# Kernel tuning notes

Hardware: AMD Instinct MI355X
Metric: run time of the kernel (lower is better)

## Reference

```python
import jax, jax.numpy as jnp
import numpy as np

NUM_LATENTS = 32768
NUM_EMBEDDINGS = 1024
EMBEDDING_SIZE = 64


def setup_inputs() -> dict:
    key = jax.random.key(0)
    kx, ke = jax.random.split(key)
    x = jax.random.normal(kx, (NUM_LATENTS * EMBEDDING_SIZE,), dtype=jnp.float32)
    # uniform init in [-limit, limit], limit = sqrt(3/embedding_size) as in the torch module
    limit = float(np.sqrt(3.0 / EMBEDDING_SIZE))
    embeddings = jax.random.uniform(
        ke, (NUM_EMBEDDINGS, EMBEDDING_SIZE), dtype=jnp.float32,
        minval=-limit, maxval=limit)
    return {"x": x, "embeddings": embeddings}


def reference(x, embeddings):
    K, E = embeddings.shape
    x_ = x.reshape(-1, E)  # [L, E]
    # squared distances ||x - e||^2 expanded: faithful to sum((x-e)**2, -1), fused as one GEMM
    d = (
        jnp.sum(x_ * x_, axis=-1, keepdims=True)
        - 2.0 * jnp.einsum('le,ke->lk', x_, embeddings)
        + jnp.sum(embeddings * embeddings, axis=-1)
    )  # [L, K]
    indices = jnp.argmin(d, axis=-1)          # [L]
    quantized = embeddings[indices].reshape(-1)  # [L*E]
    # straight-through estimator: x + (q - stop_grad(x))
    z_hat = x + quantized - jax.lax.stop_gradient(x)
    # outputs mirror the torch dict: z_continuous, z_quantized, z_hat, z_indices
    return x, quantized, z_hat, indices
```

## Files before the change

### kernel.cpp

```cpp
#include <hip/hip_runtime.h>

#define L_TOTAL   32768
#define E_DIM     64
#define K_TOTAL   1024
#define NT_TOTAL  64
#define OUT_STRIDE 2097152
#define XPAD      68

#define NT_WORDS  1280

typedef _Float16 half_t;
typedef _Float16 half8  __attribute__((ext_vector_type(8)));
typedef float    floatx4 __attribute__((ext_vector_type(4)));

__global__ __launch_bounds__(128)
void vq_swizzle_kernel(const float* __restrict__ emb, float* __restrict__ ebuf) {
    __shared__ float s_p[128];
    __shared__ float s_n[16];
    const int nt   = blockIdx.x;
    const int t    = threadIdx.x;
    const int kt   = t >> 6;
    const int lane = t & 63;
    const int q    = lane >> 4;
    const int ln   = lane & 15;

    const float* src = emb + (size_t)(nt * 16 + ln) * E_DIM + kt * 32 + q * 8;
    float4 v0 = *(const float4*)src;
    float4 v1 = *(const float4*)(src + 4);
    float f[8] = {v0.x, v0.y, v0.z, v0.w, v1.x, v1.y, v1.z, v1.w};

    half8 h, l;
    float s = 0.f;
    #pragma unroll
    for (int j = 0; j < 8; ++j) {
        half_t hh = (half_t)f[j];
        half_t ll = (half_t)(f[j] - (float)hh);
        h[j] = hh;
        l[j] = ll;
        s = fmaf(f[j], f[j], s);
    }
    float* rec = ebuf + (size_t)nt * NT_WORDS;
    *(half8*)(rec + kt * 256 + lane * 4)       = h;
    *(half8*)(rec + 512 + kt * 256 + lane * 4) = l;

    s_p[t] = s;
    __syncthreads();
    if (t < 16) {
        float n = 0.f;
        #pragma unroll
        for (int u = 0; u < 8; ++u)
            n += s_p[(u >> 2) * 64 + (u & 3) * 16 + t];
        s_n[t] = n;
    }
    __syncthreads();
    if (t < 64) rec[1024 + t] = s_n[t & 15];
}

__global__ __launch_bounds__(256, 4)
void vq_fused_kernel(const float* __restrict__ x,
                     const float* __restrict__ emb,
                     const float* __restrict__ ebuf,
                     float* __restrict__ out) {
    __shared__ float s_x[32 * XPAD];
    __shared__ float s_best[4][32];
    __shared__ int   s_bidx[4][32];
    __shared__ int   s_fin[32];

    const int tid   = threadIdx.x;
    const int ks    = tid >> 6;
    const int lane  = tid & 63;
    const int q     = lane >> 4;
    const int ln    = lane & 15;
    const int mbase = blockIdx.x * 32;
    const int rot   = blockIdx.x & 15;
    const int nt0   = ks * 16;

    {
        const float4* xg = (const float4*)(x + (size_t)mbase * E_DIM);
        #pragma unroll
        for (int i = 0; i < 2; ++i) {
            const int f   = i * 256 + tid;
            const int row = f >> 4;
            const int col = (f & 15) * 4;
            *(float4*)(&s_x[row * XPAD + col]) = xg[f];
        }
    }
    __syncthreads();

    half8 A[2][2][2];
    floatx4 xq[2];
    #pragma unroll
    for (int rt = 0; rt < 2; ++rt) {
        const float* xr = &s_x[(rt * 16 + ln) * XPAD + q * 8];
        float sn = 0.f;
        #pragma unroll
        for (int kt = 0; kt < 2; ++kt) {
            float4 v0 = *(const float4*)(xr + kt * 32);
            float4 v1 = *(const float4*)(xr + kt * 32 + 4);
            float f[8] = {v0.x, v0.y, v0.z, v0.w, v1.x, v1.y, v1.z, v1.w};
            #pragma unroll
            for (int j = 0; j < 8; ++j) {
                half_t hh = (half_t)f[j];
                half_t ll = (half_t)(f[j] - (float)hh);
                A[rt][kt][0][j] = hh;
                A[rt][kt][1][j] = ll;
                sn = fmaf(f[j], f[j], sn);
            }
        }
        sn += __shfl_xor(sn, 16, 64);
        sn += __shfl_xor(sn, 32, 64);
        #pragma unroll
        for (int r = 0; r < 4; ++r)
            xq[rt][r] = __shfl(sn, q * 4 + r, 64);
    }

    float best[2][4];
    int   bidx[2][4];
    #pragma unroll
    for (int rt = 0; rt < 2; ++rt)
        #pragma unroll
        for (int r = 0; r < 4; ++r) { best[rt][r] = 3.402823466e+38f; bidx[rt][r] = 0x7fffffff; }

    half8 a0, a1, a2, a3; float ae;
    half8 b0, b1, b2, b3; float be;
    int nt_a, nt_b;
    {
        nt_a = nt0 + rot;
        nt_a = nt0 + (rot & 15);
        nt_a = nt0 + ((0 + rot) & 15);
        const float* rec = ebuf + (size_t)nt_a * NT_WORDS;
        a0 = *(const half8*)(rec + lane * 4);
        a1 = *(const half8*)(rec + 256 + lane * 4);
        a2 = *(const half8*)(rec + 512 + lane * 4);
        a3 = *(const half8*)(rec + 768 + lane * 4);
        ae = rec[1024 + lane];
    }

    #pragma unroll 1
    for (int j = 0; j < 16; j += 2) {
        nt_b = nt0 + ((j + 1 + rot) & 15);
        {
            const float* rec = ebuf + (size_t)nt_b * NT_WORDS;
            b0 = *(const half8*)(rec + lane * 4);
            b1 = *(const half8*)(rec + 256 + lane * 4);
            b2 = *(const half8*)(rec + 512 + lane * 4);
            b3 = *(const half8*)(rec + 768 + lane * 4);
            be = rec[1024 + lane];
        }
        {
            const int kg = nt_a * 16 + ln;
            #pragma unroll
            for (int rt = 0; rt < 2; ++rt) {
                floatx4 Ca = {0.f, 0.f, 0.f, 0.f};
                floatx4 Cb = {0.f, 0.f, 0.f, 0.f};
                Ca = __builtin_amdgcn_mfma_f32_16x16x32_f16(A[rt][0][0], a0, Ca, 0, 0, 0);
                Ca = __builtin_amdgcn_mfma_f32_16x16x32_f16(A[rt][1][0], a1, Ca, 0, 0, 0);
                Cb = __builtin_amdgcn_mfma_f32_16x16x32_f16(A[rt][0][1], a0, Cb, 0, 0, 0);
                Cb = __builtin_amdgcn_mfma_f32_16x16x32_f16(A[rt][1][1], a1, Cb, 0, 0, 0);
                Cb = __builtin_amdgcn_mfma_f32_16x16x32_f16(A[rt][0][0], a2, Cb, 0, 0, 0);
                Cb = __builtin_amdgcn_mfma_f32_16x16x32_f16(A[rt][1][0], a3, Cb, 0, 0, 0);
                #pragma unroll
                for (int r = 0; r < 4; ++r) {
                    float dot = Ca[r] + Cb[r];
                    float d = __fadd_rn(__fsub_rn(xq[rt][r], __fmul_rn(2.0f, dot)), ae);
                    if (d < best[rt][r] || (d == best[rt][r] && kg < bidx[rt][r])) {
                        best[rt][r] = d; bidx[rt][r] = kg;
                    }
                }
            }
        }
        if (j + 2 < 16) {
            nt_a = nt0 + ((j + 2 + rot) & 15);
            const float* rec = ebuf + (size_t)nt_a * NT_WORDS;
            a0 = *(const half8*)(rec + lane * 4);
            a1 = *(const half8*)(rec + 256 + lane * 4);
            a2 = *(const half8*)(rec + 512 + lane * 4);
            a3 = *(const half8*)(rec + 768 + lane * 4);
            ae = rec[1024 + lane];
        }
        {
            const int kg = nt_b * 16 + ln;
            #pragma unroll
            for (int rt = 0; rt < 2; ++rt) {
                floatx4 Ca = {0.f, 0.f, 0.f, 0.f};
                floatx4 Cb = {0.f, 0.f, 0.f, 0.f};
                Ca = __builtin_amdgcn_mfma_f32_16x16x32_f16(A[rt][0][0], b0, Ca, 0, 0, 0);
                Ca = __builtin_amdgcn_mfma_f32_16x16x32_f16(A[rt][1][0], b1, Ca, 0, 0, 0);
                Cb = __builtin_amdgcn_mfma_f32_16x16x32_f16(A[rt][0][1], b0, Cb, 0, 0, 0);
                Cb = __builtin_amdgcn_mfma_f32_16x16x32_f16(A[rt][1][1], b1, Cb, 0, 0, 0);
                Cb = __builtin_amdgcn_mfma_f32_16x16x32_f16(A[rt][0][0], b2, Cb, 0, 0, 0);
                Cb = __builtin_amdgcn_mfma_f32_16x16x32_f16(A[rt][1][0], b3, Cb, 0, 0, 0);
                #pragma unroll
                for (int r = 0; r < 4; ++r) {
                    float dot = Ca[r] + Cb[r];
                    float d = __fadd_rn(__fsub_rn(xq[rt][r], __fmul_rn(2.0f, dot)), be);
                    if (d < best[rt][r] || (d == best[rt][r] && kg < bidx[rt][r])) {
                        best[rt][r] = d; bidx[rt][r] = kg;
                    }
                }
            }
        }
    }

    #pragma unroll
    for (int o = 1; o < 16; o <<= 1) {
        #pragma unroll
        for (int rt = 0; rt < 2; ++rt)
            #pragma unroll
            for (int r = 0; r < 4; ++r) {
                float ob = __shfl_xor(best[rt][r], o, 64);
                int   oi = __shfl_xor(bidx[rt][r], o, 64);
                if (ob < best[rt][r] || (ob == best[rt][r] && oi < bidx[rt][r])) {
                    best[rt][r] = ob; bidx[rt][r] = oi;
                }
            }
    }
    if (ln == 0) {
        #pragma unroll
        for (int rt = 0; rt < 2; ++rt)
            #pragma unroll
            for (int r = 0; r < 4; ++r) {
                s_best[ks][rt * 16 + q * 4 + r] = best[rt][r];
                s_bidx[ks][rt * 16 + q * 4 + r] = bidx[rt][r];
            }
    }
    __syncthreads();

    if (tid < 32) {
        float b = 3.402823466e+38f;
        int   i = 0x7fffffff;
        #pragma unroll
        for (int s = 0; s < 4; ++s) {
            float pb = s_best[s][tid];
            int   pi = s_bidx[s][tid];
            if (pb < b || (pb == b && pi < i)) { b = pb; i = pi; }
        }
        s_fin[tid] = i;
        out[3 * (size_t)OUT_STRIDE + mbase + tid] = (float)i;
    }
    __syncthreads();

    {
        const size_t fb = (size_t)mbase * (E_DIM / 4);
        float4* o0 = (float4*)out + fb;
        float4* o1 = (float4*)(out + OUT_STRIDE) + fb;
        float4* o2 = (float4*)(out + 2 * (size_t)OUT_STRIDE) + fb;
        #pragma unroll
        for (int i = 0; i < 2; ++i) {
            const int f   = i * 256 + tid;
            const int row = f >> 4;
            const int col = (f & 15) * 4;
            const float4 xv = *(const float4*)(&s_x[row * XPAD + col]);
            const int idx = s_fin[row];
            const float4 qv = *(const float4*)(emb + (size_t)idx * E_DIM + col);
            float4 z;
            z.x = __fsub_rn(__fadd_rn(xv.x, qv.x), xv.x);
            z.y = __fsub_rn(__fadd_rn(xv.y, qv.y), xv.y);
            z.z = __fsub_rn(__fadd_rn(xv.z, qv.z), xv.z);
            z.w = __fsub_rn(__fadd_rn(xv.w, qv.w), xv.w);
            o0[f] = xv;
            o1[f] = qv;
            o2[f] = z;
        }
    }
}

extern "C" void kernel_launch(void* const* d_in, const int* in_sizes, int n_in,
                              void* d_out, int out_size, void* d_ws, size_t ws_size,
                              hipStream_t stream) {
    const float* x   = (const float*)d_in[0];
    const float* emb = (const float*)d_in[1];
    float* out  = (float*)d_out;
    float* ebuf = (float*)d_ws;

    hipLaunchKernelGGL(vq_swizzle_kernel, dim3(NT_TOTAL), dim3(128), 0, stream,
                       emb, ebuf);
    hipLaunchKernelGGL(vq_fused_kernel, dim3(L_TOTAL / 32), dim3(256), 0, stream,
                       x, emb, ebuf, out);
}
```

Before: 88.79 us.

## Drop per-row norm from argmin and split running minimum by codebook order

```diff
diff --git a/kernel.cpp b/kernel.cpp
--- a/kernel.cpp
+++ b/kernel.cpp
@@ -13,8 +13,10 @@
 typedef _Float16 half8  __attribute__((ext_vector_type(8)));
 typedef float    floatx4 __attribute__((ext_vector_type(4)));
 
+__device__ float g_ebuf[NT_TOTAL * NT_WORDS];
+
 __global__ __launch_bounds__(128)
-void vq_swizzle_kernel(const float* __restrict__ emb, float* __restrict__ ebuf) {
+void vq_swizzle_kernel(const float* __restrict__ emb) {
     __shared__ float s_p[128];
     __shared__ float s_n[16];
     const int nt   = blockIdx.x;
@@ -39,7 +41,7 @@
         l[j] = ll;
         s = fmaf(f[j], f[j], s);
     }
-    float* rec = ebuf + (size_t)nt * NT_WORDS;
+    float* rec = g_ebuf + (size_t)nt * NT_WORDS;
     *(half8*)(rec + kt * 256 + lane * 4)       = h;
     *(half8*)(rec + 512 + kt * 256 + lane * 4) = l;
 
@@ -56,10 +58,50 @@
     if (t < 64) rec[1024 + t] = s_n[t & 15];
 }
 
+
+#define MFMA16(Af, Bf, C) \
+    C = __builtin_amdgcn_mfma_f32_16x16x32_f16(Af, Bf, C, 0, 0, 0)
+
+#define COMPUTE_NT(r0, r1, r2, r3, rn, NTv, Tv)                               \
+    {                                                                         \
+        const int kg_ = (NTv) * 16 + ln;                                      \
+        floatx4 k0_, k1_;                                                     \
+        {                                                                     \
+            floatx4 Ca = {0.f,0.f,0.f,0.f}, Cb = {0.f,0.f,0.f,0.f};           \
+            MFMA16(A[0][0][0], r0, Ca); MFMA16(A[0][1][0], r1, Ca);           \
+            MFMA16(A[0][0][1], r0, Cb); MFMA16(A[0][1][1], r1, Cb);           \
+            MFMA16(A[0][0][0], r2, Cb); MFMA16(A[0][1][0], r3, Cb);           \
+            _Pragma("unroll")                                                 \
+            for (int r = 0; r < 4; ++r)                                       \
+                k0_[r] = fmaf(-2.0f, Ca[r] + Cb[r], rn);                      \
+        }                                                                     \
+        {                                                                     \
+            floatx4 Ca = {0.f,0.f,0.f,0.f}, Cb = {0.f,0.f,0.f,0.f};           \
+            MFMA16(A[1][0][0], r0, Ca); MFMA16(A[1][1][0], r1, Ca);           \
+            MFMA16(A[1][0][1], r0, Cb); MFMA16(A[1][1][1], r1, Cb);           \
+            MFMA16(A[1][0][0], r2, Cb); MFMA16(A[1][1][0], r3, Cb);           \
+            _Pragma("unroll")                                                 \
+            for (int r = 0; r < 4; ++r)                                       \
+                k1_[r] = fmaf(-2.0f, Ca[r] + Cb[r], rn);                      \
+        }                                                                     \
+        if ((Tv) < c) {             \
+            _Pragma("unroll")                                                 \
+            for (int r = 0; r < 4; ++r) {                                     \
+                if (k0_[r] < bH[0][r]) { bH[0][r] = k0_[r]; iH[0][r] = kg_; } \
+                if (k1_[r] < bH[1][r]) { bH[1][r] = k1_[r]; iH[1][r] = kg_; } \
+            }                                                                 \
+        } else {                                \
+            _Pragma("unroll")                                                 \
+            for (int r = 0; r < 4; ++r) {                                     \
+                if (k0_[r] < bL[0][r]) { bL[0][r] = k0_[r]; iL[0][r] = kg_; } \
+                if (k1_[r] < bL[1][r]) { bL[1][r] = k1_[r]; iL[1][r] = kg_; } \
+            }                                                                 \
+        }                                                                     \
+    }
+
 __global__ __launch_bounds__(256, 4)
 void vq_fused_kernel(const float* __restrict__ x,
                      const float* __restrict__ emb,
-                     const float* __restrict__ ebuf,
                      float* __restrict__ out) {
     __shared__ float s_x[32 * XPAD];
     __shared__ float s_best[4][32];
@@ -74,6 +116,7 @@
     const int mbase = blockIdx.x * 32;
     const int rot   = blockIdx.x & 15;
     const int nt0   = ks * 16;
+    const int c     = 16 - rot;
 
     {
         const float4* xg = (const float4*)(x + (size_t)mbase * E_DIM);
@@ -88,11 +131,9 @@
     __syncthreads();
 
     half8 A[2][2][2];
-    floatx4 xq[2];
     #pragma unroll
     for (int rt = 0; rt < 2; ++rt) {
         const float* xr = &s_x[(rt * 16 + ln) * XPAD + q * 8];
-        float sn = 0.f;
         #pragma unroll
         for (int kt = 0; kt < 2; ++kt) {
             float4 v0 = *(const float4*)(xr + kt * 32);
@@ -104,31 +145,26 @@
                 half_t ll = (half_t)(f[j] - (float)hh);
                 A[rt][kt][0][j] = hh;
                 A[rt][kt][1][j] = ll;
-                sn = fmaf(f[j], f[j], sn);
             }
         }
-        sn += __shfl_xor(sn, 16, 64);
-        sn += __shfl_xor(sn, 32, 64);
-        #pragma unroll
-        for (int r = 0; r < 4; ++r)
-            xq[rt][r] = __shfl(sn, q * 4 + r, 64);
-    }
-
-    float best[2][4];
-    int   bidx[2][4];
+    }
+
+    float bH[2][4], bL[2][4];
+    int   iH[2][4], iL[2][4];
     #pragma unroll
     for (int rt = 0; rt < 2; ++rt)
         #pragma unroll
-        for (int r = 0; r < 4; ++r) { best[rt][r] = 3.402823466e+38f; bidx[rt][r] = 0x7fffffff; }
+        for (int r = 0; r < 4; ++r) {
+            bH[rt][r] = 3.402823466e+38f; iH[rt][r] = 0x7fffffff;
+            bL[rt][r] = 3.402823466e+38f; iL[rt][r] = 0x7fffffff;
+        }
 
     half8 a0, a1, a2, a3; float ae;
     half8 b0, b1, b2, b3; float be;
     int nt_a, nt_b;
     {
-        nt_a = nt0 + rot;
         nt_a = nt0 + (rot & 15);
-        nt_a = nt0 + ((0 + rot) & 15);
-        const float* rec = ebuf + (size_t)nt_a * NT_WORDS;
+        const float* rec = g_ebuf + (size_t)nt_a * NT_WORDS;
         a0 = *(const half8*)(rec + lane * 4);
         a1 = *(const half8*)(rec + 256 + lane * 4);
         a2 = *(const half8*)(rec + 512 + lane * 4);
@@ -137,70 +173,38 @@
     }
 
     #pragma unroll 1
-    for (int j = 0; j < 16; j += 2) {
-        nt_b = nt0 + ((j + 1 + rot) & 15);
+    for (int t = 0; t < 16; t += 2) {
+        nt_b = nt0 + ((t + 1 + rot) & 15);
         {
-            const float* rec = ebuf + (size_t)nt_b * NT_WORDS;
+            const float* rec = g_ebuf + (size_t)nt_b * NT_WORDS;
             b0 = *(const half8*)(rec + lane * 4);
             b1 = *(const half8*)(rec + 256 + lane * 4);
             b2 = *(const half8*)(rec + 512 + lane * 4);
             b3 = *(const half8*)(rec + 768 + lane * 4);
             be = rec[1024 + lane];
         }
-        {
-            const int kg = nt_a * 16 + ln;
-            #pragma unroll
-            for (int rt = 0; rt < 2; ++rt) {
-                floatx4 Ca = {0.f, 0.f, 0.f, 0.f};
-                floatx4 Cb = {0.f, 0.f, 0.f, 0.f};
-                Ca = __builtin_amdgcn_mfma_f32_16x16x32_f16(A[rt][0][0], a0, Ca, 0, 0, 0);
-                Ca = __builtin_amdgcn_mfma_f32_16x16x32_f16(A[rt][1][0], a1, Ca, 0, 0, 0);
-                Cb = __builtin_amdgcn_mfma_f32_16x16x32_f16(A[rt][0][1], a0, Cb, 0, 0, 0);
-                Cb = __builtin_amdgcn_mfma_f32_16x16x32_f16(A[rt][1][1], a1, Cb, 0, 0, 0);
-                Cb = __builtin_amdgcn_mfma_f32_16x16x32_f16(A[rt][0][0], a2, Cb, 0, 0, 0);
-                Cb = __builtin_amdgcn_mfma_f32_16x16x32_f16(A[rt][1][0], a3, Cb, 0, 0, 0);
-                #pragma unroll
-                for (int r = 0; r < 4; ++r) {
-                    float dot = Ca[r] + Cb[r];
-                    float d = __fadd_rn(__fsub_rn(xq[rt][r], __fmul_rn(2.0f, dot)), ae);
-                    if (d < best[rt][r] || (d == best[rt][r] && kg < bidx[rt][r])) {
-                        best[rt][r] = d; bidx[rt][r] = kg;
-                    }
-                }
-            }
-        }
-        if (j + 2 < 16) {
-            nt_a = nt0 + ((j + 2 + rot) & 15);
-            const float* rec = ebuf + (size_t)nt_a * NT_WORDS;
+        COMPUTE_NT(a0, a1, a2, a3, ae, nt_a, t);
+        if (t + 2 < 16) {
+            nt_a = nt0 + ((t + 2 + rot) & 15);
+            const float* rec = g_ebuf + (size_t)nt_a * NT_WORDS;
             a0 = *(const half8*)(rec + lane * 4);
             a1 = *(const half8*)(rec + 256 + lane * 4);
             a2 = *(const half8*)(rec + 512 + lane * 4);
             a3 = *(const half8*)(rec + 768 + lane * 4);
             ae = rec[1024 + lane];
         }
-        {
-            const int kg = nt_b * 16 + ln;
-            #pragma unroll
-            for (int rt = 0; rt < 2; ++rt) {
-                floatx4 Ca = {0.f, 0.f, 0.f, 0.f};
-                floatx4 Cb = {0.f, 0.f, 0.f, 0.f};
-                Ca = __builtin_amdgcn_mfma_f32_16x16x32_f16(A[rt][0][0], b0, Ca, 0, 0, 0);
-                Ca = __builtin_amdgcn_mfma_f32_16x16x32_f16(A[rt][1][0], b1, Ca, 0, 0, 0);
-                Cb = __builtin_amdgcn_mfma_f32_16x16x32_f16(A[rt][0][1], b0, Cb, 0, 0, 0);
-                Cb = __builtin_amdgcn_mfma_f32_16x16x32_f16(A[rt][1][1], b1, Cb, 0, 0, 0);
-                Cb = __builtin_amdgcn_mfma_f32_16x16x32_f16(A[rt][0][0], b2, Cb, 0, 0, 0);
-                Cb = __builtin_amdgcn_mfma_f32_16x16x32_f16(A[rt][1][0], b3, Cb, 0, 0, 0);
-                #pragma unroll
-                for (int r = 0; r < 4; ++r) {
-                    float dot = Ca[r] + Cb[r];
-                    float d = __fadd_rn(__fsub_rn(xq[rt][r], __fmul_rn(2.0f, dot)), be);
-                    if (d < best[rt][r] || (d == best[rt][r] && kg < bidx[rt][r])) {
-                        best[rt][r] = d; bidx[rt][r] = kg;
-                    }
-                }
-            }
-        }
-    }
+        COMPUTE_NT(b0, b1, b2, b3, be, nt_b, t + 1);
+    }
+
+    float best[2][4];
+    int   bidx[2][4];
+    #pragma unroll
+    for (int rt = 0; rt < 2; ++rt)
+        #pragma unroll
+        for (int r = 0; r < 4; ++r) {
+            if (bL[rt][r] <= bH[rt][r]) { best[rt][r] = bL[rt][r]; bidx[rt][r] = iL[rt][r]; }
+            else                        { best[rt][r] = bH[rt][r]; bidx[rt][r] = iH[rt][r]; }
+        }
 
     #pragma unroll
     for (int o = 1; o < 16; o <<= 1) {
@@ -271,10 +275,10 @@
     const float* x   = (const float*)d_in[0];
     const float* emb = (const float*)d_in[1];
     float* out  = (float*)d_out;
-    float* ebuf = (float*)d_ws;
+    (void)d_ws; (void)ws_size;
 
     hipLaunchKernelGGL(vq_swizzle_kernel, dim3(NT_TOTAL), dim3(128), 0, stream,
-                       emb, ebuf);
+                       emb);
     hipLaunchKernelGGL(vq_fused_kernel, dim3(L_TOTAL / 32), dim3(256), 0, stream,
-                       x, emb, ebuf, out);
+                       x, emb, out);
 }
```

After: 88.62 us. No clear change (-0.2%).
